# Kernel tuning notes

Hardware: AMD Instinct MI355X
Metric: run time of the kernel (lower is better)

The kernel has to match this reference:

```python
import jax, jax.numpy as jnp
import numpy as np

N_QUBITS = 12
N_LAYERS = 4
BATCH = 256

# State is kept as shape (batch, 2, 2, ..., 2) with qubit q on axis q+1.
# Z(0) measures the first qubit axis.

def _apply_1q(psi, q, U):
    """Apply a shared 2x2 gate U to qubit q."""
    p = jnp.moveaxis(psi, q + 1, -1)
    p = jnp.einsum('ij,...j->...i', U.astype(psi.dtype), p)
    return jnp.moveaxis(p, -1, q + 1)


def _rz_batch(psi, q, theta):
    """RZ with per-sample angle theta of shape (batch,). RZ = diag(e^{-i t/2}, e^{i t/2})."""
    half = 0.5 * theta
    ph = jnp.stack([jnp.exp(-1j * half), jnp.exp(1j * half)], axis=-1)  # (b, 2)
    ph = ph.reshape((theta.shape[0],) + (1,) * (N_QUBITS - 1) + (2,)).astype(psi.dtype)
    p = jnp.moveaxis(psi, q + 1, -1)
    return jnp.moveaxis(p * ph, -1, q + 1)


def _rz_shared(psi, q, theta):
    """RZ with a scalar (weight) angle shared across the batch."""
    half = 0.5 * theta
    ph = jnp.stack([jnp.exp(-1j * half), jnp.exp(1j * half)]).astype(psi.dtype)  # (2,)
    p = jnp.moveaxis(psi, q + 1, -1)
    return jnp.moveaxis(p * ph, -1, q + 1)


def _ry(psi, q, theta):
    """RY(theta) = [[cos(t/2), -sin(t/2)], [sin(t/2), cos(t/2)]], scalar angle."""
    c, s = jnp.cos(0.5 * theta), jnp.sin(0.5 * theta)
    U = jnp.stack([jnp.stack([c, -s]), jnp.stack([s, c])])
    return _apply_1q(psi, q, U)


def _cx(psi, c, t):
    """CNOT with control c, target t: flip target where control == 1."""
    p = jnp.moveaxis(psi, (c + 1, t + 1), (-2, -1))
    p = jnp.stack([p[..., 0, :], p[..., 1, ::-1]], axis=-2)
    return jnp.moveaxis(p, (-2, -1), (c + 1, t + 1))


def _forward(x, weights):
    b = x.shape[0]
    # H on every qubit starting from |0...0> -> uniform superposition.
    psi = jnp.full((b,) + (2,) * N_QUBITS, np.float32(2.0 ** (-N_QUBITS / 2.0)),
                   dtype=jnp.complex64)
    w = weights.reshape(N_LAYERS, N_QUBITS, 2)  # (layer, qubit, [ry, rz])
    for l in range(N_LAYERS):
        for q in range(N_QUBITS):                 # data re-uploading encoding
            psi = _rz_batch(psi, q, x[:, q])
        for q in range(N_QUBITS):                 # trainable rotations
            psi = _ry(psi, q, w[l, q, 0])
            psi = _rz_shared(psi, q, w[l, q, 1])
        for q in range(N_QUBITS - 1):             # entangling ladder
            psi = _cx(psi, q, q + 1)
    # <Z(0)> = P(qubit0 = 0) - P(qubit0 = 1)
    pr = jnp.sum(jnp.abs(psi) ** 2, axis=tuple(range(2, N_QUBITS + 1)))  # (b, 2)
    return (pr[:, 0] - pr[:, 1])[:, None]  # (b, 1) float32


def setup_inputs() -> dict:
    key = jax.random.key(0)
    kx, kw = jax.random.split(key)
    x = jax.random.normal(kx, (BATCH, N_QUBITS), dtype=jnp.float32)
    weights = jax.random.uniform(kw, (2 * N_LAYERS * N_QUBITS,),
                                 dtype=jnp.float32) * np.float32(2.0 * np.pi)
    return {"x": x, "weights": weights}


def reference(x, weights):
    return _forward(x, weights)
```

## Files before the change

### kernel.cpp

```cpp
#include <hip/hip_runtime.h>

#define NQ 12
#define NL 4
#define DIM 4096
#define BLOCK 512
#define PER_T 8
#define BATCH 256


__device__ __forceinline__ float2 cmul(float2 a, float2 b) {
    return make_float2(a.x * b.x - a.y * b.y, a.x * b.y + a.y * b.x);
}
__device__ __forceinline__ float2 cconj(float2 a) { return make_float2(a.x, -a.y); }

__device__ __forceinline__ float2 fsincos(float ang) {
    float r = ang * 0.15915494309189535f;
    r = r - floorf(r);
    return make_float2(__builtin_amdgcn_cosf(r), __builtin_amdgcn_sinf(r));
}

template <int CTRL>
__device__ __forceinline__ float dppx(float v) {
    int i = __builtin_bit_cast(int, v);
    int r = __builtin_amdgcn_update_dpp(0, i, CTRL, 0xF, 0xF, true);
    return __builtin_bit_cast(float, r);
}
template <int MSK, int CTRL>
__device__ __forceinline__ void ry_dpp(float2* psi, int lane, float c, float s) {
    const float se = (lane & MSK) ? s : -s;
#pragma unroll
    for (int k = 0; k < PER_T; ++k) {
        float px = dppx<CTRL>(psi[k].x);
        float py = dppx<CTRL>(psi[k].y);
        psi[k].x = c * psi[k].x + se * px;
        psi[k].y = c * psi[k].y + se * py;
    }
}
__device__ __forceinline__ void ry_dpp4(float2* psi, int lane, float c, float s) {
    const float se = (lane & 4) ? s : -s;
#pragma unroll
    for (int k = 0; k < PER_T; ++k) {
        float px = dppx<0x1B>(dppx<0x141>(psi[k].x));
        float py = dppx<0x1B>(dppx<0x141>(psi[k].y));
        psi[k].x = c * psi[k].x + se * px;
        psi[k].y = c * psi[k].y + se * py;
    }
}

__global__ __launch_bounds__(BLOCK, 2) void qcp_kernel(
    const float* __restrict__ x,
    const float* __restrict__ w,
    float* __restrict__ out)
{
    __shared__ float2 sP[DIM];
    __shared__ float2 sQ[DIM];
    __shared__ float2 trig[NL * NQ * 2];
    __shared__ float  zhalf[NL * NQ];
    __shared__ float  rbuf[8];

    const int b    = blockIdx.x;
    const int t    = threadIdx.x;
    const int lane = t & 63;
    const int wv   = t >> 6;

    if (t < NL * NQ * 2) trig[t] = fsincos(0.5f * w[t]);
    if (t < NL * NQ) zhalf[t] = 0.5f * w[2 * t + 1];

    float xr[NQ];
#pragma unroll
    for (int q = 0; q < NQ; ++q) xr[q] = x[b * NQ + q];

    int iA[PER_T], iB[PER_T], gI[PER_T];
#pragma unroll
    for (int k = 0; k < PER_T; ++k) {
        iA[k] = lane | (k << 6) | (wv << 9);
        iB[k] = lane | (wv << 6) | (k << 9);
        gI[k] = iA[k] ^ (iA[k] >> 1);
    }

    float2 eph[PER_T];
#pragma unroll
    for (int k = 0; k < PER_T; ++k) {
        int j = iA[k];
        float ang = 0.0f;
#pragma unroll
        for (int q = 0; q < NQ; ++q)
            ang += ((j >> (NQ - 1 - q)) & 1) ? 0.5f * xr[q] : -0.5f * xr[q];
        eph[k] = fsincos(ang);
    }

    float2 psi[PER_T];
#pragma unroll
    for (int k = 0; k < PER_T; ++k) psi[k] = make_float2(0.015625f, 0.0f);

    __syncthreads();

    for (int l = 0; l < NL; ++l) {
        float2 tRY[9];
        float2 tRY0[3], tZ0[3];
        float  zh[4];
        float2 z3, z4, z5;
        float2 z6, z7;
#pragma unroll
        for (int q = 3; q <= 11; ++q) tRY[q - 3] = trig[(l * NQ + q) * 2];
#pragma unroll
        for (int q = 0; q < 3; ++q) {
            tRY0[q] = trig[(l * NQ + q) * 2 + 0];
            tZ0[q]  = trig[(l * NQ + q) * 2 + 1];
        }
        z3 = trig[(l * NQ + 3) * 2 + 1];
        z4 = trig[(l * NQ + 4) * 2 + 1];
        z5 = trig[(l * NQ + 5) * 2 + 1];
        z6 = trig[(l * NQ + 6) * 2 + 1];
        z7 = trig[(l * NQ + 7) * 2 + 1];
#pragma unroll
        for (int q = 8; q <= 11; ++q) zh[q - 8] = zhalf[l * NQ + q];

#pragma unroll
        for (int k = 0; k < PER_T; ++k) psi[k] = cmul(psi[k], eph[k]);

#pragma unroll
        for (int q = 3; q <= 5; ++q) {
            const int kb = (11 - q) - 6;
            float c = tRY[q - 3].x, s = tRY[q - 3].y;
#pragma unroll
            for (int m = 0; m < PER_T / 2; ++m) {
                int k0 = ((m >> kb) << (kb + 1)) | (m & ((1 << kb) - 1));
                int k1 = k0 | (1 << kb);
                float2 a0 = psi[k0], a1 = psi[k1];
                psi[k0] = make_float2(c * a0.x - s * a1.x, c * a0.y - s * a1.y);
                psi[k1] = make_float2(s * a0.x + c * a1.x, s * a0.y + c * a1.y);
            }
        }

        ry_dpp<8, 0x128>(psi, lane, tRY[5].x, tRY[5].y);
        ry_dpp4(psi, lane, tRY[6].x, tRY[6].y);
        ry_dpp<2, 0x4E>(psi, lane, tRY[7].x, tRY[7].y);
        ry_dpp<1, 0xB1>(psi, lane, tRY[8].x, tRY[8].y);

        float s_lane = 0.0f;
#pragma unroll
        for (int p = 0; p < 4; ++p)
            s_lane += ((lane >> p) & 1) ? zh[3 - p] : -zh[3 - p];
        {
            float2 base = fsincos(s_lane);
            float2 z45[4];
#pragma unroll
            for (int c2 = 0; c2 < 4; ++c2) {
                float2 a4 = (c2 & 2) ? z4 : cconj(z4);
                float2 a5 = (c2 & 1) ? z5 : cconj(z5);
                z45[c2] = cmul(a4, a5);
            }
#pragma unroll
            for (int k = 0; k < PER_T; ++k) {
                float2 a3 = (k & 4) ? z3 : cconj(z3);
                float2 ph = cmul(cmul(base, a3), z45[k & 3]);
                psi[k] = cmul(psi[k], ph);
            }
        }

#pragma unroll
        for (int k = 0; k < PER_T; ++k) sP[iA[k]] = psi[k];

        const int  b6  = (lane >> 5) & 1;
        const float c6 = tRY[3].x;
        const float se6 = b6 ? tRY[3].y : -tRY[3].y;
        const float2 zb6 = b6 ? z6 : cconj(z6);
        __syncthreads();
#pragma unroll
        for (int k = 0; k < PER_T; ++k) {
            float2 own = sP[iB[k]];
            float2 oth = sP[iB[k] ^ 32];
            float2 n = make_float2(c6 * own.x + se6 * oth.x,
                                   c6 * own.y + se6 * oth.y);
            psi[k] = cmul(n, zb6);
        }

#pragma unroll
        for (int q = 0; q < 3; ++q) {
            const int kb = 2 - q;
            float c = tRY0[q].x, s = tRY0[q].y;
            float2 z = tZ0[q];
#pragma unroll
            for (int m = 0; m < PER_T / 2; ++m) {
                int k0 = ((m >> kb) << (kb + 1)) | (m & ((1 << kb) - 1));
                int k1 = k0 | (1 << kb);
                float2 a0 = psi[k0], a1 = psi[k1];
                float2 n0 = make_float2(c * a0.x - s * a1.x, c * a0.y - s * a1.y);
                float2 n1 = make_float2(s * a0.x + c * a1.x, s * a0.y + c * a1.y);
                psi[k0] = cmul(n0, cconj(z));
                psi[k1] = cmul(n1, z);
            }
        }

#pragma unroll
        for (int k = 0; k < PER_T; ++k) sQ[iB[k]] = psi[k];

        const int  b7  = ((lane >> 4) ^ (lane >> 5)) & 1;
        const float c7 = tRY[4].x;
        const float se7 = b7 ? tRY[4].y : -tRY[4].y;
        const float2 zb7 = b7 ? z7 : cconj(z7);
        __syncthreads();
#pragma unroll
        for (int k = 0; k < PER_T; ++k) {
            float2 own = sQ[gI[k]];
            float2 oth = sQ[gI[k] ^ 16];
            float2 n = make_float2(c7 * own.x + se7 * oth.x,
                                   c7 * own.y + se7 * oth.y);
            psi[k] = cmul(n, zb7);
        }
    }

    float acc = 0.0f;
#pragma unroll
    for (int k = 0; k < PER_T; ++k)
        acc += psi[k].x * psi[k].x + psi[k].y * psi[k].y;
    if (wv >= 4) acc = -acc;
#pragma unroll
    for (int off = 32; off > 0; off >>= 1)
        acc += __shfl_down(acc, off, 64);
    if (lane == 0) rbuf[wv] = acc;
    __syncthreads();
    if (t == 0) {
        float tot = 0.0f;
#pragma unroll
        for (int i = 0; i < 8; ++i) tot += rbuf[i];
        out[b] = tot;
    }
}

extern "C" void kernel_launch(void* const* d_in, const int* in_sizes, int n_in,
                              void* d_out, int out_size, void* d_ws, size_t ws_size,
                              hipStream_t stream) {
    const float* x = (const float*)d_in[0];
    const float* w = (const float*)d_in[1];
    float* out = (float*)d_out;
    qcp_kernel<<<BATCH, BLOCK, 0, stream>>>(x, w, out);
}
```

Measured before the change: 68.88 us.

## Truncate final layer to Z0 light cone and fuse last two cross-wave gates

Runs two full layers, then a third layer in which the qubit-6 and qubit-7 shared-memory exchanges are merged into one 4-point read, skipping the second transpose and its barrier. The fourth layer is replaced by an analytic expectation of Z on qubit 0, written as a closed-form combination of populations and coherences over the qubit-0/qubit-1/qubit-2 amplitudes that stay in registers. This drops most of the last layer's gate work and one sync per layer, at the cost of relying on the light-cone algebra being exactly right for this circuit structure.

```diff
diff --git a/kernel.cpp b/kernel.cpp
--- a/kernel.cpp
+++ b/kernel.cpp
@@ -95,12 +95,11 @@
 
     __syncthreads();
 
-    for (int l = 0; l < NL; ++l) {
+    for (int l = 0; l < 2; ++l) {
         float2 tRY[9];
         float2 tRY0[3], tZ0[3];
         float  zh[4];
-        float2 z3, z4, z5;
-        float2 z6, z7;
+        float2 z3, z4, z5, z6, z7;
 #pragma unroll
         for (int q = 3; q <= 11; ++q) tRY[q - 3] = trig[(l * NQ + q) * 2];
 #pragma unroll
@@ -161,9 +160,8 @@
 
 #pragma unroll
         for (int k = 0; k < PER_T; ++k) sP[iA[k]] = psi[k];
-
-        const int  b6  = (lane >> 5) & 1;
-        const float c6 = tRY[3].x;
+        const int   b6  = (lane >> 5) & 1;
+        const float c6  = tRY[3].x;
         const float se6 = b6 ? tRY[3].y : -tRY[3].y;
         const float2 zb6 = b6 ? z6 : cconj(z6);
         __syncthreads();
@@ -195,9 +193,8 @@
 
 #pragma unroll
         for (int k = 0; k < PER_T; ++k) sQ[iB[k]] = psi[k];
-
-        const int  b7  = ((lane >> 4) ^ (lane >> 5)) & 1;
-        const float c7 = tRY[4].x;
+        const int   b7  = ((lane >> 4) ^ (lane >> 5)) & 1;
+        const float c7  = tRY[4].x;
         const float se7 = b7 ? tRY[4].y : -tRY[4].y;
         const float2 zb7 = b7 ? z7 : cconj(z7);
         __syncthreads();
@@ -211,11 +208,130 @@
         }
     }
 
-    float acc = 0.0f;
-#pragma unroll
-    for (int k = 0; k < PER_T; ++k)
-        acc += psi[k].x * psi[k].x + psi[k].y * psi[k].y;
-    if (wv >= 4) acc = -acc;
+    {
+        const int l = 2;
+        float2 tRY[9];
+        float2 tRY0[3], tZ0[3];
+        float  zh[4];
+        float2 z3, z4, z5, z6, z7;
+#pragma unroll
+        for (int q = 3; q <= 11; ++q) tRY[q - 3] = trig[(l * NQ + q) * 2];
+#pragma unroll
+        for (int q = 0; q < 3; ++q) {
+            tRY0[q] = trig[(l * NQ + q) * 2 + 0];
+            tZ0[q]  = trig[(l * NQ + q) * 2 + 1];
+        }
+        z3 = trig[(l * NQ + 3) * 2 + 1];
+        z4 = trig[(l * NQ + 4) * 2 + 1];
+        z5 = trig[(l * NQ + 5) * 2 + 1];
+        z6 = trig[(l * NQ + 6) * 2 + 1];
+        z7 = trig[(l * NQ + 7) * 2 + 1];
+#pragma unroll
+        for (int q = 8; q <= 11; ++q) zh[q - 8] = zhalf[l * NQ + q];
+
+#pragma unroll
+        for (int k = 0; k < PER_T; ++k) psi[k] = cmul(psi[k], eph[k]);
+
+#pragma unroll
+        for (int q = 3; q <= 5; ++q) {
+            const int kb = (11 - q) - 6;
+            float c = tRY[q - 3].x, s = tRY[q - 3].y;
+#pragma unroll
+            for (int m = 0; m < PER_T / 2; ++m) {
+                int k0 = ((m >> kb) << (kb + 1)) | (m & ((1 << kb) - 1));
+                int k1 = k0 | (1 << kb);
+                float2 a0 = psi[k0], a1 = psi[k1];
+                psi[k0] = make_float2(c * a0.x - s * a1.x, c * a0.y - s * a1.y);
+                psi[k1] = make_float2(s * a0.x + c * a1.x, s * a0.y + c * a1.y);
+            }
+        }
+
+        ry_dpp<8, 0x128>(psi, lane, tRY[5].x, tRY[5].y);
+        ry_dpp4(psi, lane, tRY[6].x, tRY[6].y);
+        ry_dpp<2, 0x4E>(psi, lane, tRY[7].x, tRY[7].y);
+        ry_dpp<1, 0xB1>(psi, lane, tRY[8].x, tRY[8].y);
+
+        float s_lane = 0.0f;
+#pragma unroll
+        for (int p = 0; p < 4; ++p)
+            s_lane += ((lane >> p) & 1) ? zh[3 - p] : -zh[3 - p];
+        {
+            float2 base = fsincos(s_lane);
+            float2 z45[4];
+#pragma unroll
+            for (int c2 = 0; c2 < 4; ++c2) {
+                float2 a4 = (c2 & 2) ? z4 : cconj(z4);
+                float2 a5 = (c2 & 1) ? z5 : cconj(z5);
+                z45[c2] = cmul(a4, a5);
+            }
+#pragma unroll
+            for (int k = 0; k < PER_T; ++k) {
+                float2 a3 = (k & 4) ? z3 : cconj(z3);
+                float2 ph = cmul(cmul(base, a3), z45[k & 3]);
+                psi[k] = cmul(psi[k], ph);
+            }
+        }
+
+#pragma unroll
+        for (int k = 0; k < PER_T; ++k) sP[iA[k]] = psi[k];
+        const int b6 = (lane >> 5) & 1;
+        const int b7 = (lane >> 4) & 1;
+        const float c6v = tRY[3].x, s6 = tRY[3].y;
+        const float c7v = tRY[4].x, s7 = tRY[4].y;
+        const float r6c0 = b6 ? s6 : c6v,  r6c1 = b6 ? c6v : -s6;
+        const float r7c0 = b7 ? s7 : c7v,  r7c1 = b7 ? c7v : -s7;
+        const float w00 = r6c0 * r7c0, w01 = r6c0 * r7c1;
+        const float w10 = r6c1 * r7c0, w11 = r6c1 * r7c1;
+        const float2 zb67 = cmul(b6 ? z6 : cconj(z6), b7 ? z7 : cconj(z7));
+        __syncthreads();
+#pragma unroll
+        for (int k = 0; k < PER_T; ++k) {
+            int base = iB[k] & ~0x30;
+            float2 v00 = sP[base];
+            float2 v01 = sP[base | 0x10];
+            float2 v10 = sP[base | 0x20];
+            float2 v11 = sP[base | 0x30];
+            float nx = w00 * v00.x + w01 * v01.x + w10 * v10.x + w11 * v11.x;
+            float ny = w00 * v00.y + w01 * v01.y + w10 * v10.y + w11 * v11.y;
+            psi[k] = cmul(make_float2(nx, ny), zb67);
+        }
+
+#pragma unroll
+        for (int q = 0; q < 3; ++q) {
+            const int kb = 2 - q;
+            float c = tRY0[q].x, s = tRY0[q].y;
+            float2 z = tZ0[q];
+#pragma unroll
+            for (int m = 0; m < PER_T / 2; ++m) {
+                int k0 = ((m >> kb) << (kb + 1)) | (m & ((1 << kb) - 1));
+                int k1 = k0 | (1 << kb);
+                float2 a0 = psi[k0], a1 = psi[k1];
+                float2 n0 = make_float2(c * a0.x - s * a1.x, c * a0.y - s * a1.y);
+                float2 n1 = make_float2(s * a0.x + c * a1.x, s * a0.y + c * a1.y);
+                psi[k0] = cmul(n0, cconj(z));
+                psi[k1] = cmul(n1, z);
+            }
+        }
+    }
+
+    float diff = 0.0f, cross = 0.0f;
+    {
+        float2 e0 = fsincos(xr[0]);
+#pragma unroll
+        for (int k = 0; k < 4; ++k) {
+            float2 a0 = psi[k];
+            float2 a1 = psi[k ^ 6];
+            diff += (a0.x * a0.x + a0.y * a0.y) - (a1.x * a1.x + a1.y * a1.y);
+            float px = a0.x * a1.x + a0.y * a1.y;
+            float py = a0.y * a1.x - a0.x * a1.y;
+            cross += px * e0.x + py * e0.y;
+        }
+    }
+    float2 t30 = trig[(3 * NQ + 0) * 2];
+    float costh = t30.x * t30.x - t30.y * t30.y;
+    float sinth = 2.0f * t30.x * t30.y;
+    float acc = costh * diff - 2.0f * sinth * cross;
+
 #pragma unroll
     for (int off = 32; off > 0; off >>= 1)
         acc += __shfl_down(acc, off, 64);
```

Result: faster. 62.76 us (-8.9%).
